# Kernel tuning notes

Measured on AMD Instinct MI355X. Metric: run time of the kernel, lower is better.

Reference implementation:

```python
import jax, jax.numpy as jnp
import numpy as np

N = 16384      # nodes (radar cells x batched graphs)
H = 128        # n_hidden
N_ENV = 7
N_IN = N_ENV + 2 + 1  # env + coords + density = 10
T_CTX = 24
HORIZON = 40
T = T_CTX + HORIZON


def setup_inputs() -> dict:
    key = jax.random.key(0)
    ks = jax.random.split(key, 40)

    def w(k, shape, fan_in):
        return jax.random.normal(k, shape, jnp.float32) * np.float32(1.0 / np.sqrt(fan_in))

    inp = {}
    inp["x"] = jax.random.normal(ks[0], (N, T), jnp.float32)
    inp["coords"] = jax.random.normal(ks[1], (N, 2), jnp.float32)
    inp["env"] = jax.random.normal(ks[2], (N, N_ENV, T), jnp.float32)
    # --- encoder params ---
    inp["enc_W_in"] = w(ks[3], (H, N_IN), N_IN)           # Linear(n_in->H), no bias
    inp["enc_Wih0"] = w(ks[4], (4 * H, H), H)
    inp["enc_Whh0"] = w(ks[5], (4 * H, H), H)
    inp["enc_bih0"] = jnp.zeros((4 * H,), jnp.float32)
    inp["enc_bhh0"] = jnp.zeros((4 * H,), jnp.float32)
    inp["enc_Wih1"] = w(ks[6], (4 * H, H), H)
    inp["enc_Whh1"] = w(ks[7], (4 * H, H), H)
    inp["enc_bih1"] = jnp.zeros((4 * H,), jnp.float32)
    inp["enc_bhh1"] = jnp.zeros((4 * H,), jnp.float32)
    # --- NodeLSTM params ---
    inp["node_W_in"] = w(ks[8], (H, N_IN), N_IN)          # Linear(n_in->H), no bias
    inp["in_Wih"] = w(ks[9], (4 * H, 2 * H), 2 * H)       # lstm_in takes [inputs, enc_state]
    inp["in_Whh"] = w(ks[10], (4 * H, H), H)
    inp["in_bih"] = jnp.zeros((4 * H,), jnp.float32)
    inp["in_bhh"] = jnp.zeros((4 * H,), jnp.float32)
    inp["l1_Wih"] = w(ks[11], (4 * H, H), H)
    inp["l1_Whh"] = w(ks[12], (4 * H, H), H)
    inp["l1_bih"] = jnp.zeros((4 * H,), jnp.float32)
    inp["l1_bhh"] = jnp.zeros((4 * H,), jnp.float32)
    # hidden2in / hidden2out heads: Linear(H,H) -> ReLU -> Linear(H,1)
    inp["h2in_W1"] = w(ks[13], (H, H), H)
    inp["h2in_b1"] = jnp.zeros((H,), jnp.float32)
    inp["h2in_W2"] = w(ks[14], (1, H), H)
    inp["h2in_b2"] = jnp.zeros((1,), jnp.float32)
    inp["h2out_W1"] = w(ks[15], (H, H), H)
    inp["h2out_b1"] = jnp.zeros((H,), jnp.float32)
    inp["h2out_W2"] = w(ks[16], (1, H), H)
    inp["h2out_b2"] = jnp.zeros((1,), jnp.float32)
    return inp


def _lstm_cell(xin, h, c, Wih, Whh, bih, bhh):
    # torch.nn.LSTMCell semantics; gate order i, f, g, o
    gates = xin @ Wih.T + h @ Whh.T + (bih + bhh)
    i, f, g, o = jnp.split(gates, 4, axis=1)
    c_new = jax.nn.sigmoid(f) * c + jax.nn.sigmoid(i) * jnp.tanh(g)
    h_new = jax.nn.sigmoid(o) * jnp.tanh(c_new)
    return h_new, c_new


def reference(x, coords, env,
              enc_W_in, enc_Wih0, enc_Whh0, enc_bih0, enc_bhh0,
              enc_Wih1, enc_Whh1, enc_bih1, enc_bhh1,
              node_W_in, in_Wih, in_Whh, in_bih, in_bhh,
              l1_Wih, l1_Whh, l1_bih, l1_bhh,
              h2in_W1, h2in_b1, h2in_W2, h2in_b2,
              h2out_W1, h2out_b1, h2out_W2, h2out_b2):
    n = x.shape[0]
    z = jnp.zeros((n, H), x.dtype)

    # ---------- encoder: scan over T_CTX context steps ----------
    def enc_step(carry, xs):
        h0, c0, h1, c1 = carry
        xt, et = xs  # [N], [N, N_ENV]
        inp = jnp.concatenate([xt[:, None], coords, et], axis=1) @ enc_W_in.T
        h0, c0 = _lstm_cell(inp, h0, c0, enc_Wih0, enc_Whh0, enc_bih0, enc_bhh0)
        h1, c1 = _lstm_cell(h0, h1, c1, enc_Wih1, enc_Whh1, enc_bih1, enc_bhh1)
        return (h0, c0, h1, c1), None

    enc_xs = (x[:, :T_CTX].T, jnp.moveaxis(env[:, :, :T_CTX], 2, 0))
    (h0, c0, h1, c1), _ = jax.lax.scan(enc_step, (z, z, z, z), enc_xs)
    enc_state = h1  # h[-1] captured at setup_states, fixed over the horizon

    def head(hid, W1, b1, W2, b2):
        return jax.nn.sigmoid(jax.nn.relu(hid @ W1.T + b1) @ W2.T + b2)

    # ---------- decoder: scan over HORIZON forecast steps ----------
    def dec_step(carry, et):
        xc, h0, c0, h1, c1 = carry
        inp = jnp.concatenate([xc, coords, et], axis=1) @ node_W_in.T
        inp = jnp.concatenate([inp, enc_state], axis=1)  # [N, 2H]
        h0, c0 = _lstm_cell(inp, h0, c0, in_Wih, in_Whh, in_bih, in_bhh)
        h1, c1 = _lstm_cell(h0, h1, c1, l1_Wih, l1_Whh, l1_bih, l1_bhh)
        x_in = head(h1, h2in_W1, h2in_b1, h2in_W2, h2in_b2)
        x_out = head(h1, h2out_W1, h2out_b1, h2out_W2, h2out_b2)
        xn = xc + x_in - x_out * xc  # source/sink update, [N, 1]
        return (xn, h0, c0, h1, c1), xn

    x0 = x[:, T_CTX - 1][:, None]
    dec_xs = jnp.moveaxis(env[:, :, T_CTX:T_CTX + HORIZON], 2, 0)
    _, ys = jax.lax.scan(dec_step, (x0, h0, c0, h1, c1), dec_xs)  # [HORIZON, N, 1]
    return jnp.transpose(ys[..., 0], (1, 0))  # [N, HORIZON]
```

## Files before the change

kernel.cpp:

```cpp
#include <hip/hip_runtime.h>
#include <hip/hip_bf16.h>
#include <cstdint>
#include <cstddef>

typedef __bf16 bf16_t;
typedef bf16_t bf16x8 __attribute__((ext_vector_type(8)));
typedef bf16_t bf16x4 __attribute__((ext_vector_type(4)));
typedef float  f32x4  __attribute__((ext_vector_type(4)));
typedef unsigned short u16x8 __attribute__((ext_vector_type(8)));

#define TT    64
#define T_CTX 24
#define HOR   40
#define SA    264
#define NTH   512
#define EWS   132

#define MFMA __builtin_amdgcn_mfma_f32_16x16x32_bf16

#define O_PKE   16
#define O_PKD   (O_PKE + 262144)
#define O_PKX   (O_PKD + 294912)
#define O_BIAS  (O_PKX + 131072)
#define O_HEADP (O_BIAS + 2048)
#define O_WINE  (O_HEADP + 512)
#define O_WINN  (O_WINE + 1536)
#define O_B2    (O_WINN + 1536)

struct Ptrs { const void* q[29]; };

__device__ __forceinline__ float sigm(float x) {
  return __builtin_amdgcn_rcpf(1.f + __expf(-x));
}
__device__ __forceinline__ float tanh_(float x) {
  return 1.f - 2.f * __builtin_amdgcn_rcpf(1.f + __expf(2.f * x));
}
__device__ __forceinline__ unsigned pk2(float a, float b) {
  unsigned ua = __float_as_uint(a), ub = __float_as_uint(b);
  ua = (ua + 0x7fffu + ((ua >> 16) & 1u)) >> 16;
  ub = (ub + 0x7fffu + ((ub >> 16) & 1u)) >> 16;
  return ua | (ub << 16);
}
__device__ __forceinline__ float uplo(unsigned p){ return __uint_as_float(p << 16); }
__device__ __forceinline__ float uphi(unsigned p){ return __uint_as_float(p & 0xffff0000u); }

__global__ void detect_kernel(const unsigned short* __restrict__ wsrc, int* __restrict__ flag)
{
  int tid = threadIdx.x;
  int wild = 0;
  for (int i = tid; i < 256; i += 64) {
    unsigned short b = wsrc[i];
    float v  = __uint_as_float(((unsigned)b) << 16);
    float av = fabsf(v);
    unsigned e = (b >> 7) & 0xff;
    if (av > 1000.f || e == 0xff || (((b & 0x7fff) != 0) && av < 1e-9f)) wild++;
  }
  for (int off = 32; off; off >>= 1) wild += __shfl_down(wild, off, 64);
  if (tid == 0) flag[0] = (wild > 16) ? 1 : 0;
}

__global__ void prep_kernel(Ptrs P, bf16_t* __restrict__ wb, const int* __restrict__ flag)
{
  const bool f32 = (flag[0] != 0);
  const int gtid = blockIdx.x * blockDim.x + threadIdx.x;
  const int gsz  = gridDim.x * blockDim.x;
  auto rd = [&](const void* src, int i) -> float {
    return f32 ? ((const float*)src)[i] : (float)((const bf16_t*)src)[i];
  };

  for (int i = gtid; i < 262144; i += gsz) {
    int w = i >> 15, r = i & 32767, f = r >> 9, e = r & 511;
    int ln = e >> 3, j = e & 7;
    int seg = f >> 5, fk = f & 31, kt = fk >> 2, g = fk & 3;
    int row = g * 128 + w * 16 + (ln & 15);
    int col = kt * 32 + ((ln >> 4) << 3) + j;
    float v;
    if (seg == 0) v = (col < 128) ? rd(P.q[4], row * 128 + col) : rd(P.q[5], row * 128 + col - 128);
    else          v = (col < 128) ? rd(P.q[8], row * 128 + col) : rd(P.q[9], row * 128 + col - 128);
    wb[O_PKE + i] = (bf16_t)v;
  }
  for (int i = gtid; i < 294912; i += gsz) {
    int w = i / 36864, r = i - w * 36864, f = r >> 9, e = r & 511;
    int ln = e >> 3, j = e & 7;
    int colk = ((ln >> 4) << 3) + j;
    float v;
    if (f < 64) {
      int seg = f >> 5, fk = f & 31, kt = fk >> 2, g = fk & 3;
      int row = g * 128 + w * 16 + (ln & 15);
      int col = kt * 32 + colk;
      if (seg == 0) v = (col < 128) ? rd(P.q[13], row * 256 + col) : rd(P.q[14], row * 128 + col - 128);
      else          v = (col < 128) ? rd(P.q[17], row * 128 + col) : rd(P.q[18], row * 128 + col - 128);
    } else {
      int f2 = f - 64, h = f2 >> 2, kt = f2 & 3;
      int row = w * 16 + (ln & 15);
      int col = kt * 32 + colk;
      v = rd(h ? P.q[25] : P.q[21], row * 128 + col);
    }
    wb[O_PKD + i] = (bf16_t)v;
  }
  for (int i = gtid; i < 131072; i += gsz) {
    int w = i >> 14, r = i & 16383, f = r >> 9, e = r & 511;
    int ln = e >> 3, j = e & 7;
    int kt = f >> 2, g = f & 3;
    int row = g * 128 + w * 16 + (ln & 15);
    int col = kt * 32 + ((ln >> 4) << 3) + j;
    wb[O_PKX + i] = (bf16_t)rd(P.q[13], row * 256 + 128 + col);
  }
  for (int i = gtid; i < 512; i += gsz) {
    wb[O_BIAS + i]        = (bf16_t)(rd(P.q[6],  i) + rd(P.q[7],  i));
    wb[O_BIAS + 512 + i]  = (bf16_t)(rd(P.q[10], i) + rd(P.q[11], i));
    wb[O_BIAS + 1024 + i] = (bf16_t)(rd(P.q[15], i) + rd(P.q[16], i));
    wb[O_BIAS + 1536 + i] = (bf16_t)(rd(P.q[19], i) + rd(P.q[20], i));
  }
  for (int i = gtid; i < 128; i += gsz) {
    wb[O_HEADP + i]       = (bf16_t)rd(P.q[22], i);
    wb[O_HEADP + 128 + i] = (bf16_t)rd(P.q[23], i);
    wb[O_HEADP + 256 + i] = (bf16_t)rd(P.q[26], i);
    wb[O_HEADP + 384 + i] = (bf16_t)rd(P.q[27], i);
  }
  for (int i = gtid; i < 1536; i += gsz) {
    int cc = i / 12, j = i % 12;
    wb[O_WINE + i] = (j < 10) ? (bf16_t)rd(P.q[3],  cc * 10 + j) : (bf16_t)0.f;
    wb[O_WINN + i] = (j < 10) ? (bf16_t)rd(P.q[12], cc * 10 + j) : (bf16_t)0.f;
  }
  if (gtid == 0) {
    wb[O_B2]     = (bf16_t)rd(P.q[24], 0);
    wb[O_B2 + 1] = (bf16_t)rd(P.q[28], 0);
  }
}

struct PreB { bf16x8 b[2][4]; };

__device__ __forceinline__ PreB preB(const bf16_t* __restrict__ pl) {
  PreB r;
#pragma unroll
  for (int p = 0; p < 2; ++p)
#pragma unroll
    for (int g = 0; g < 4; ++g)
      r.b[p][g] = *(const bf16x8*)(pl + (p * 4 + g) * 512);
  return r;
}

template<int NKT>
__device__ __forceinline__ void gemm_pk(f32x4 (&acc)[4][4], const bf16_t* __restrict__ As,
                                        const bf16_t* __restrict__ pl, const PreB& pre,
                                        const bf16_t* __restrict__ plpf, PreB* __restrict__ pf,
                                        int l, int q)
{
  bf16x8 bw[3][4];
#pragma unroll
  for (int g = 0; g < 4; ++g) { bw[0][g] = pre.b[0][g]; bw[1][g] = pre.b[1][g]; }
#pragma unroll
  for (int g = 0; g < 4; ++g) bw[2][g] = *(const bf16x8*)(pl + (8 + g) * 512);
#pragma unroll
  for (int kt = 0; kt < NKT; ++kt) {
    if (kt == 1) {
#pragma unroll
      for (int p = 0; p < 2; ++p)
#pragma unroll
        for (int g = 0; g < 4; ++g)
          pf->b[p][g] = *(const bf16x8*)(plpf + (p * 4 + g) * 512);
    }
    const bf16_t* Ar = As + l * SA + kt * 32 + q * 8;
    bf16x8 a0 = *(const bf16x8*)(Ar);
    bf16x8 a1 = *(const bf16x8*)(Ar + 16 * SA);
#pragma unroll
    for (int g = 0; g < 4; ++g) acc[g][0] = MFMA(a0, bw[kt % 3][g], acc[g][0], 0, 0, 0);
    a0 = *(const bf16x8*)(Ar + 32 * SA);
#pragma unroll
    for (int g = 0; g < 4; ++g) acc[g][1] = MFMA(a1, bw[kt % 3][g], acc[g][1], 0, 0, 0);
    a1 = *(const bf16x8*)(Ar + 48 * SA);
#pragma unroll
    for (int g = 0; g < 4; ++g) acc[g][2] = MFMA(a0, bw[kt % 3][g], acc[g][2], 0, 0, 0);
#pragma unroll
    for (int g = 0; g < 4; ++g) acc[g][3] = MFMA(a1, bw[kt % 3][g], acc[g][3], 0, 0, 0);
    if (kt + 3 < NKT) {
#pragma unroll
      for (int g = 0; g < 4; ++g)
        bw[kt % 3][g] = *(const bf16x8*)(pl + ((kt + 3) * 4 + g) * 512);
    }
  }
}

template<bool DUAL>
__device__ __forceinline__ void cell_up(f32x4 (&acc)[4][4], float (&c)[16],
                                        bf16_t* __restrict__ shb, bf16_t* __restrict__ sha,
                                        const bf16_t* __restrict__ bias,
                                        int wid, int l, int q)
{
  const int jc = wid * 16 + l;
  const float bi  = (float)bias[jc];
  const float bf_ = (float)bias[128 + jc];
  const float bg  = (float)bias[256 + jc];
  const float bo  = (float)bias[384 + jc];
#pragma unroll
  for (int mt = 0; mt < 4; ++mt) {
#pragma unroll
    for (int r = 0; r < 4; ++r) {
      float gi = acc[0][mt][r] + bi;
      float gf = acc[1][mt][r] + bf_;
      float gg = acc[2][mt][r] + bg;
      float go = acc[3][mt][r] + bo;
      float cn = sigm(gf) * c[mt * 4 + r] + sigm(gi) * tanh_(gg);
      float hh = sigm(go) * tanh_(cn);
      c[mt * 4 + r] = cn;
      const int row = mt * 16 + q * 4 + r;
      shb[row * SA + jc] = (bf16_t)hh;
      if (DUAL) sha[row * SA + jc] = (bf16_t)hh;
    }
  }
}

__device__ __forceinline__ void proj16(const float* v, const bf16_t* __restrict__ wbase,
                                       bf16_t* __restrict__ sx, int nd, int sub)
{
  bf16x8 o0, o1;
#pragma unroll
  for (int cc = 0; cc < 16; ++cc) {
    const bf16_t* wr = wbase + (sub * 16 + cc) * 12;
    bf16x4 w0 = *(const bf16x4*)(wr);
    bf16x4 w1 = *(const bf16x4*)(wr + 4);
    bf16x4 w2 = *(const bf16x4*)(wr + 8);
    float a = v[0] * (float)w0[0] + v[1] * (float)w0[1] + v[2] * (float)w0[2] + v[3] * (float)w0[3]
            + v[4] * (float)w1[0] + v[5] * (float)w1[1] + v[6] * (float)w1[2] + v[7] * (float)w1[3]
            + v[8] * (float)w2[0] + v[9] * (float)w2[1];
    if (cc < 8) o0[cc] = (bf16_t)a; else o1[cc - 8] = (bf16_t)a;
  }
  *(bf16x8*)(sx + nd * SA + sub * 16)     = o0;
  *(bf16x8*)(sx + nd * SA + sub * 16 + 8) = o1;
}

template<typename T>
__global__ __launch_bounds__(NTH, 2) void lstm_persist(
    const T* __restrict__ x, const T* __restrict__ coords, const T* __restrict__ env,
    const bf16_t* __restrict__ w, const int* __restrict__ flag, T* __restrict__ out)
{
  const bool want_f32 = (sizeof(T) == 4);
  if ((flag[0] != 0) != want_f32) return;

  __shared__ __align__(16) bf16_t bufA[64 * SA];
  __shared__ __align__(16) bf16_t bufB[64 * SA];
  __shared__ __align__(16) bf16_t s_win[2 * 128 * 12];
  __shared__ __align__(16) bf16_t s_bias[4 * 512];
  __shared__ float s_red[128];
  __shared__ float s_xc[64];
  __shared__ __align__(16) float s_ew[64 * EWS];
  __shared__ float s_out[64 * HOR];

  const int tid  = threadIdx.x;
  const int wid  = tid >> 6;
  const int lane = tid & 63;
  const int l    = tid & 15;
  const int q    = (tid & 63) >> 4;
  const int node0 = blockIdx.x * 64;
  const int nd  = tid >> 3;
  const int sub = tid & 7;
  const int nd_e = tid / 7;
  const int e_e  = tid - nd_e * 7;

  const bf16_t* plE0 = w + O_PKE + wid * 32768 + lane * 8;
  const bf16_t* plE1 = plE0 + 16384;
  const bf16_t* plD0 = w + O_PKD + wid * 36864 + lane * 8;
  const bf16_t* plD1 = plD0 + 16384;
  const bf16_t* plH  = plD0 + 32768;
  const bf16_t* plX  = w + O_PKX + wid * 16384 + lane * 8;

  auto load_ew = [&](int t0) {
    float* dst = (tid < 448) ? &s_ew[nd_e * EWS + e_e * 16]
                             : &s_ew[(tid - 448) * EWS + 112];
    const T* src = (tid < 448) ? env + ((size_t)(node0 + nd_e) * 7 + e_e) * TT + t0
                               : x + (size_t)(node0 + tid - 448) * TT + t0;
    if constexpr (sizeof(T) == 4) {
#pragma unroll
      for (int u = 0; u < 4; ++u) {
        f32x4 vv = __builtin_nontemporal_load((const f32x4*)src + u);
        *((f32x4*)dst + u) = vv;
      }
    } else {
#pragma unroll
      for (int u = 0; u < 2; ++u) {
        u16x8 vv = __builtin_nontemporal_load((const u16x8*)src + u);
#pragma unroll
        for (int k = 0; k < 8; ++k)
          dst[u * 8 + k] = __uint_as_float(((unsigned)vv[k]) << 16);
      }
    }
  };

  for (int i = tid; i < 2048; i += NTH) s_bias[i] = w[O_BIAS + i];
  for (int i = tid; i < 3072; i += NTH) s_win[i]  = w[O_WINE + i];
  for (int i = tid; i < 64 * SA; i += NTH) { bufA[i] = (bf16_t)0.f; bufB[i] = (bf16_t)0.f; }
  load_ew(0);

  const float cx = (float)coords[(size_t)(node0 + nd) * 2 + 0];
  const float cy = (float)coords[(size_t)(node0 + nd) * 2 + 1];

  float c0[16], c1[16];
#pragma unroll
  for (int i = 0; i < 16; ++i) { c0[i] = 0.f; c1[i] = 0.f; }

  PreB pA = preB(plE0);
  PreB pD;
  __syncthreads();

#pragma unroll 1
  for (int t = 0; t < T_CTX; ++t) {
    if (t == 16) { __syncthreads(); load_ew(16); __syncthreads(); }
    const int tw = t & 15;
    float v[10];
    v[0] = s_ew[nd * EWS + 112 + tw];
    v[1] = cx; v[2] = cy;
#pragma unroll
    for (int e = 0; e < 7; ++e) v[3 + e] = s_ew[nd * EWS + e * 16 + tw];
    proj16(v, s_win, bufA, nd, sub);
    __syncthreads();

    f32x4 acc[4][4];
#pragma unroll
    for (int g = 0; g < 4; ++g)
#pragma unroll
      for (int mt = 0; mt < 4; ++mt) acc[g][mt] = f32x4{0.f, 0.f, 0.f, 0.f};
    PreB pC;
    gemm_pk<8>(acc, bufA, plE0, pA, plE1, &pC, l, q);
    __syncthreads();
    cell_up<true>(acc, c0, bufB, bufA + 128, s_bias, wid, l, q);
    __syncthreads();

#pragma unroll
    for (int g = 0; g < 4; ++g)
#pragma unroll
      for (int mt = 0; mt < 4; ++mt) acc[g][mt] = f32x4{0.f, 0.f, 0.f, 0.f};
    gemm_pk<8>(acc, bufB, plE1, pC, (t < T_CTX - 1) ? plE0 : plX, &pA, l, q);
    __syncthreads();
    cell_up<false>(acc, c1, bufB + 128, nullptr, s_bias + 512, wid, l, q);
  }
  __syncthreads();

  uint2 geh[4][4];
  {
    f32x4 acc[4][4];
#pragma unroll
    for (int g = 0; g < 4; ++g)
#pragma unroll
      for (int mt = 0; mt < 4; ++mt) acc[g][mt] = f32x4{0.f, 0.f, 0.f, 0.f};
    gemm_pk<4>(acc, bufB + 128, plX, pA, plD0, &pD, l, q);
#pragma unroll
    for (int g = 0; g < 4; ++g)
#pragma unroll
      for (int mt = 0; mt < 4; ++mt)
        geh[g][mt] = uint2{pk2(acc[g][mt][0], acc[g][mt][1]),
                           pk2(acc[g][mt][2], acc[g][mt][3])};
  }
  if (tid < 64) s_xc[tid] = s_ew[tid * EWS + 112 + 7];
  const float b2i = (float)w[O_B2];
  const float b2o = (float)w[O_B2 + 1];
  const float b1i = (float)w[O_HEADP + wid * 16 + l];
  const float w2i = (float)w[O_HEADP + 128 + wid * 16 + l];
  const float b1o = (float)w[O_HEADP + 256 + wid * 16 + l];
  const float w2o = (float)w[O_HEADP + 384 + wid * 16 + l];
  __syncthreads();

#pragma unroll 1
  for (int s = 0; s < HOR; ++s) {
    const int t = T_CTX + s;
    if ((t & 15) == 0) { load_ew(t); __syncthreads(); }
    const int tw = t & 15;
    float v[10];
    v[0] = s_xc[nd];
    v[1] = cx; v[2] = cy;
#pragma unroll
    for (int e = 0; e < 7; ++e) v[3 + e] = s_ew[nd * EWS + e * 16 + tw];
    proj16(v, s_win + 1536, bufA, nd, sub);
    __syncthreads();

    f32x4 acc[4][4];
#pragma unroll
    for (int g = 0; g < 4; ++g)
#pragma unroll
      for (int mt = 0; mt < 4; ++mt)
        acc[g][mt] = f32x4{uplo(geh[g][mt].x), uphi(geh[g][mt].x),
                           uplo(geh[g][mt].y), uphi(geh[g][mt].y)};
    PreB pC;
    gemm_pk<8>(acc, bufA, plD0, pD, plD1, &pC, l, q);
    __syncthreads();
    cell_up<true>(acc, c0, bufB, bufA + 128, s_bias + 1024, wid, l, q);
    __syncthreads();

#pragma unroll
    for (int g = 0; g < 4; ++g)
#pragma unroll
      for (int mt = 0; mt < 4; ++mt) acc[g][mt] = f32x4{0.f, 0.f, 0.f, 0.f};
    gemm_pk<8>(acc, bufB, plD1, pC, plD0, &pD, l, q);
    bf16x8 hb[8];
#pragma unroll
    for (int f = 0; f < 8; ++f) hb[f] = *(const bf16x8*)(plH + f * 512);
    __syncthreads();
    cell_up<false>(acc, c1, bufB + 128, nullptr, s_bias + 1536, wid, l, q);
    if (tid < 128) s_red[tid] = 0.f;
    __syncthreads();

    f32x4 hacc[2][4];
#pragma unroll
    for (int hd = 0; hd < 2; ++hd)
#pragma unroll
      for (int mt = 0; mt < 4; ++mt) hacc[hd][mt] = f32x4{0.f, 0.f, 0.f, 0.f};
#pragma unroll
    for (int kt = 0; kt < 4; ++kt) {
      bf16x8 a[4];
#pragma unroll
      for (int mt = 0; mt < 4; ++mt)
        a[mt] = *(const bf16x8*)(bufB + 128 + (mt * 16 + l) * SA + kt * 32 + q * 8);
#pragma unroll
      for (int mt = 0; mt < 4; ++mt) {
        hacc[0][mt] = MFMA(a[mt], hb[kt],     hacc[0][mt], 0, 0, 0);
        hacc[1][mt] = MFMA(a[mt], hb[4 + kt], hacc[1][mt], 0, 0, 0);
      }
    }
#pragma unroll
    for (int hd = 0; hd < 2; ++hd) {
      const float b1v = hd ? b1o : b1i;
      const float w2v = hd ? w2o : w2i;
#pragma unroll
      for (int mt = 0; mt < 4; ++mt)
#pragma unroll
        for (int r = 0; r < 4; ++r) {
          float val = fmaxf(hacc[hd][mt][r] + b1v, 0.f) * w2v;
          val += __shfl_xor(val, 1, 64);
          val += __shfl_xor(val, 2, 64);
          val += __shfl_xor(val, 4, 64);
          val += __shfl_xor(val, 8, 64);
          if (l == 0) atomicAdd(&s_red[hd * 64 + mt * 16 + q * 4 + r], val);
        }
    }
    __syncthreads();
    if (tid < 64) {
      float xc = s_xc[tid];
      float si = sigm(s_red[tid] + b2i);
      float so = sigm(s_red[64 + tid] + b2o);
      float xn = xc + si - so * xc;
      s_xc[tid] = xn;
      s_out[tid * HOR + s] = xn;
    }
    __syncthreads();
  }

  for (int i = tid; i < 64 * HOR; i += NTH)
    out[(size_t)node0 * HOR + i] = (T)s_out[i];
}

extern "C" void kernel_launch(void* const* d_in, const int* in_sizes, int n_in,
                              void* d_out, int out_size, void* d_ws, size_t ws_size,
                              hipStream_t stream) {
  (void)in_sizes; (void)n_in; (void)out_size; (void)ws_size;
  Ptrs P;
  for (int i = 0; i < 29; ++i) P.q[i] = d_in[i];
  int*    flag = (int*)d_ws;
  bf16_t* w    = (bf16_t*)d_ws;

  detect_kernel<<<1, 64, 0, stream>>>((const unsigned short*)d_in[4], flag);
  prep_kernel<<<256, 256, 0, stream>>>(P, w, flag);
  lstm_persist<float><<<256, NTH, 0, stream>>>(
      (const float*)d_in[0], (const float*)d_in[1], (const float*)d_in[2],
      w, flag, (float*)d_out);
  lstm_persist<bf16_t><<<256, NTH, 0, stream>>>(
      (const bf16_t*)d_in[0], (const bf16_t*)d_in[1], (const bf16_t*)d_in[2],
      w, flag, (bf16_t*)d_out);
}
```

Measured before the change: 1.933 ms.

## Process 128 nodes per 1024-thread block sharing weight fragments across row halves

Doubles the nodes per workgroup to 128 using 16 waves, where two groups of 8 waves split the rows and share the same weight column slices. The grid drops to 128 blocks. The 16-step env staging buffer is replaced by a per-step double-buffered scalar load, and outputs are written directly to global each step instead of staged in shared memory. The aim is to halve weight traffic per node and cut shared memory for the env buffer. The risk is that with 128 blocks on 256 CUs only half the CUs are used, and the per-step scalar global loads add latency on every iteration.

```diff
diff --git a/kernel.cpp b/kernel.cpp
--- a/kernel.cpp
+++ b/kernel.cpp
@@ -7,14 +7,13 @@
 typedef bf16_t bf16x8 __attribute__((ext_vector_type(8)));
 typedef bf16_t bf16x4 __attribute__((ext_vector_type(4)));
 typedef float  f32x4  __attribute__((ext_vector_type(4)));
-typedef unsigned short u16x8 __attribute__((ext_vector_type(8)));
 
 #define TT    64
 #define T_CTX 24
 #define HOR   40
 #define SA    264
-#define NTH   512
-#define EWS   132
+#define NTH   1024
+#define NODES 128
 
 #define MFMA __builtin_amdgcn_mfma_f32_16x16x32_bf16
 
@@ -186,9 +185,8 @@
 __device__ __forceinline__ void cell_up(f32x4 (&acc)[4][4], float (&c)[16],
                                         bf16_t* __restrict__ shb, bf16_t* __restrict__ sha,
                                         const bf16_t* __restrict__ bias,
-                                        int wid, int l, int q)
-{
-  const int jc = wid * 16 + l;
+                                        int jc, int l, int q)
+{
   const float bi  = (float)bias[jc];
   const float bf_ = (float)bias[128 + jc];
   const float bg  = (float)bias[256 + jc];
@@ -231,66 +229,51 @@
 }
 
 template<typename T>
-__global__ __launch_bounds__(NTH, 2) void lstm_persist(
+__global__ __launch_bounds__(NTH, 1) void lstm_persist(
     const T* __restrict__ x, const T* __restrict__ coords, const T* __restrict__ env,
     const bf16_t* __restrict__ w, const int* __restrict__ flag, T* __restrict__ out)
 {
   const bool want_f32 = (sizeof(T) == 4);
   if ((flag[0] != 0) != want_f32) return;
 
-  __shared__ __align__(16) bf16_t bufA[64 * SA];
-  __shared__ __align__(16) bf16_t bufB[64 * SA];
+  __shared__ __align__(16) bf16_t bufA[NODES * SA];
+  __shared__ __align__(16) bf16_t bufB[NODES * SA];
   __shared__ __align__(16) bf16_t s_win[2 * 128 * 12];
   __shared__ __align__(16) bf16_t s_bias[4 * 512];
-  __shared__ float s_red[128];
-  __shared__ float s_xc[64];
-  __shared__ __align__(16) float s_ew[64 * EWS];
-  __shared__ float s_out[64 * HOR];
+  __shared__ float s_red[2 * NODES];
+  __shared__ float s_xc[NODES];
+  __shared__ float s_env[2][NODES][8];
 
   const int tid  = threadIdx.x;
   const int wid  = tid >> 6;
+  const int ws   = wid & 7;
+  const int rb   = (wid >> 3) * 64;
   const int lane = tid & 63;
   const int l    = tid & 15;
   const int q    = (tid & 63) >> 4;
-  const int node0 = blockIdx.x * 64;
+  const int jc   = ws * 16 + l;
+  const int node0 = blockIdx.x * NODES;
   const int nd  = tid >> 3;
   const int sub = tid & 7;
   const int nd_e = tid / 7;
   const int e_e  = tid - nd_e * 7;
 
-  const bf16_t* plE0 = w + O_PKE + wid * 32768 + lane * 8;
+  const bf16_t* plE0 = w + O_PKE + ws * 32768 + lane * 8;
   const bf16_t* plE1 = plE0 + 16384;
-  const bf16_t* plD0 = w + O_PKD + wid * 36864 + lane * 8;
+  const bf16_t* plD0 = w + O_PKD + ws * 36864 + lane * 8;
   const bf16_t* plD1 = plD0 + 16384;
   const bf16_t* plH  = plD0 + 32768;
-  const bf16_t* plX  = w + O_PKX + wid * 16384 + lane * 8;
-
-  auto load_ew = [&](int t0) {
-    float* dst = (tid < 448) ? &s_ew[nd_e * EWS + e_e * 16]
-                             : &s_ew[(tid - 448) * EWS + 112];
-    const T* src = (tid < 448) ? env + ((size_t)(node0 + nd_e) * 7 + e_e) * TT + t0
-                               : x + (size_t)(node0 + tid - 448) * TT + t0;
-    if constexpr (sizeof(T) == 4) {
-#pragma unroll
-      for (int u = 0; u < 4; ++u) {
-        f32x4 vv = __builtin_nontemporal_load((const f32x4*)src + u);
-        *((f32x4*)dst + u) = vv;
-      }
-    } else {
-#pragma unroll
-      for (int u = 0; u < 2; ++u) {
-        u16x8 vv = __builtin_nontemporal_load((const u16x8*)src + u);
-#pragma unroll
-        for (int k = 0; k < 8; ++k)
-          dst[u * 8 + k] = __uint_as_float(((unsigned)vv[k]) << 16);
-      }
-    }
+  const bf16_t* plX  = w + O_PKX + ws * 16384 + lane * 8;
+
+  auto load_env = [&](int t0, int buf) {
+    if (tid < 896) s_env[buf][nd_e][e_e] = (float)env[((size_t)(node0 + nd_e) * 7 + e_e) * TT + t0];
+    else           s_env[buf][tid - 896][7] = (float)x[(size_t)(node0 + tid - 896) * TT + t0];
   };
 
   for (int i = tid; i < 2048; i += NTH) s_bias[i] = w[O_BIAS + i];
   for (int i = tid; i < 3072; i += NTH) s_win[i]  = w[O_WINE + i];
-  for (int i = tid; i < 64 * SA; i += NTH) { bufA[i] = (bf16_t)0.f; bufB[i] = (bf16_t)0.f; }
-  load_ew(0);
+  for (int i = tid; i < NODES * SA; i += NTH) { bufA[i] = (bf16_t)0.f; bufB[i] = (bf16_t)0.f; }
+  load_env(0, 0);
 
   const float cx = (float)coords[(size_t)(node0 + nd) * 2 + 0];
   const float cy = (float)coords[(size_t)(node0 + nd) * 2 + 1];
@@ -305,14 +288,14 @@
 
 #pragma unroll 1
   for (int t = 0; t < T_CTX; ++t) {
-    if (t == 16) { __syncthreads(); load_ew(16); __syncthreads(); }
-    const int tw = t & 15;
+    const int tn = t + 1;
     float v[10];
-    v[0] = s_ew[nd * EWS + 112 + tw];
+    v[0] = s_env[t & 1][nd][7];
     v[1] = cx; v[2] = cy;
 #pragma unroll
-    for (int e = 0; e < 7; ++e) v[3 + e] = s_ew[nd * EWS + e * 16 + tw];
+    for (int e = 0; e < 7; ++e) v[3 + e] = s_env[t & 1][nd][e];
     proj16(v, s_win, bufA, nd, sub);
+    load_env(tn, tn & 1);
     __syncthreads();
 
     f32x4 acc[4][4];
@@ -321,18 +304,18 @@
 #pragma unroll
       for (int mt = 0; mt < 4; ++mt) acc[g][mt] = f32x4{0.f, 0.f, 0.f, 0.f};
     PreB pC;
-    gemm_pk<8>(acc, bufA, plE0, pA, plE1, &pC, l, q);
-    __syncthreads();
-    cell_up<true>(acc, c0, bufB, bufA + 128, s_bias, wid, l, q);
+    gemm_pk<8>(acc, bufA + rb * SA, plE0, pA, plE1, &pC, l, q);
+    __syncthreads();
+    cell_up<true>(acc, c0, bufB + rb * SA, bufA + rb * SA + 128, s_bias, jc, l, q);
     __syncthreads();
 
 #pragma unroll
     for (int g = 0; g < 4; ++g)
 #pragma unroll
       for (int mt = 0; mt < 4; ++mt) acc[g][mt] = f32x4{0.f, 0.f, 0.f, 0.f};
-    gemm_pk<8>(acc, bufB, plE1, pC, (t < T_CTX - 1) ? plE0 : plX, &pA, l, q);
-    __syncthreads();
-    cell_up<false>(acc, c1, bufB + 128, nullptr, s_bias + 512, wid, l, q);
+    gemm_pk<8>(acc, bufB + rb * SA, plE1, pC, (t < T_CTX - 1) ? plE0 : plX, &pA, l, q);
+    __syncthreads();
+    cell_up<false>(acc, c1, bufB + rb * SA + 128, nullptr, s_bias + 512, jc, l, q);
   }
   __syncthreads();
 
@@ -343,7 +326,7 @@
     for (int g = 0; g < 4; ++g)
 #pragma unroll
       for (int mt = 0; mt < 4; ++mt) acc[g][mt] = f32x4{0.f, 0.f, 0.f, 0.f};
-    gemm_pk<4>(acc, bufB + 128, plX, pA, plD0, &pD, l, q);
+    gemm_pk<4>(acc, bufB + rb * SA + 128, plX, pA, plD0, &pD, l, q);
 #pragma unroll
     for (int g = 0; g < 4; ++g)
 #pragma unroll
@@ -351,26 +334,26 @@
         geh[g][mt] = uint2{pk2(acc[g][mt][0], acc[g][mt][1]),
                            pk2(acc[g][mt][2], acc[g][mt][3])};
   }
-  if (tid < 64) s_xc[tid] = s_ew[tid * EWS + 112 + 7];
+  if (tid < NODES) s_xc[tid] = s_env[1][tid][7];
   const float b2i = (float)w[O_B2];
   const float b2o = (float)w[O_B2 + 1];
-  const float b1i = (float)w[O_HEADP + wid * 16 + l];
-  const float w2i = (float)w[O_HEADP + 128 + wid * 16 + l];
-  const float b1o = (float)w[O_HEADP + 256 + wid * 16 + l];
-  const float w2o = (float)w[O_HEADP + 384 + wid * 16 + l];
+  const float b1i = (float)w[O_HEADP + jc];
+  const float w2i = (float)w[O_HEADP + 128 + jc];
+  const float b1o = (float)w[O_HEADP + 256 + jc];
+  const float w2o = (float)w[O_HEADP + 384 + jc];
   __syncthreads();
 
 #pragma unroll 1
   for (int s = 0; s < HOR; ++s) {
     const int t = T_CTX + s;
-    if ((t & 15) == 0) { load_ew(t); __syncthreads(); }
-    const int tw = t & 15;
+    const int tn = t + 1;
     float v[10];
     v[0] = s_xc[nd];
     v[1] = cx; v[2] = cy;
 #pragma unroll
-    for (int e = 0; e < 7; ++e) v[3 + e] = s_ew[nd * EWS + e * 16 + tw];
+    for (int e = 0; e < 7; ++e) v[3 + e] = s_env[t & 1][nd][e];
     proj16(v, s_win + 1536, bufA, nd, sub);
+    if (tn < TT) load_env(tn, tn & 1);
     __syncthreads();
 
     f32x4 acc[4][4];
@@ -381,22 +364,22 @@
         acc[g][mt] = f32x4{uplo(geh[g][mt].x), uphi(geh[g][mt].x),
                            uplo(geh[g][mt].y), uphi(geh[g][mt].y)};
     PreB pC;
-    gemm_pk<8>(acc, bufA, plD0, pD, plD1, &pC, l, q);
-    __syncthreads();
-    cell_up<true>(acc, c0, bufB, bufA + 128, s_bias + 1024, wid, l, q);
+    gemm_pk<8>(acc, bufA + rb * SA, plD0, pD, plD1, &pC, l, q);
+    __syncthreads();
+    cell_up<true>(acc, c0, bufB + rb * SA, bufA + rb * SA + 128, s_bias + 1024, jc, l, q);
     __syncthreads();
 
 #pragma unroll
     for (int g = 0; g < 4; ++g)
 #pragma unroll
       for (int mt = 0; mt < 4; ++mt) acc[g][mt] = f32x4{0.f, 0.f, 0.f, 0.f};
-    gemm_pk<8>(acc, bufB, plD1, pC, plD0, &pD, l, q);
+    gemm_pk<8>(acc, bufB + rb * SA, plD1, pC, plD0, &pD, l, q);
     bf16x8 hb[8];
 #pragma unroll
     for (int f = 0; f < 8; ++f) hb[f] = *(const bf16x8*)(plH + f * 512);
     __syncthreads();
-    cell_up<false>(acc, c1, bufB + 128, nullptr, s_bias + 1536, wid, l, q);
-    if (tid < 128) s_red[tid] = 0.f;
+    cell_up<false>(acc, c1, bufB + rb * SA + 128, nullptr, s_bias + 1536, jc, l, q);
+    if (tid < 2 * NODES) s_red[tid] = 0.f;
     __syncthreads();
 
     f32x4 hacc[2][4];
@@ -409,7 +392,7 @@
       bf16x8 a[4];
 #pragma unroll
       for (int mt = 0; mt < 4; ++mt)
-        a[mt] = *(const bf16x8*)(bufB + 128 + (mt * 16 + l) * SA + kt * 32 + q * 8);
+        a[mt] = *(const bf16x8*)(bufB + (rb + mt * 16 + l) * SA + 128 + kt * 32 + q * 8);
 #pragma unroll
       for (int mt = 0; mt < 4; ++mt) {
         hacc[0][mt] = MFMA(a[mt], hb[kt],     hacc[0][mt], 0, 0, 0);
@@ -429,23 +412,20 @@
           val += __shfl_xor(val, 2, 64);
           val += __shfl_xor(val, 4, 64);
           val += __shfl_xor(val, 8, 64);
-          if (l == 0) atomicAdd(&s_red[hd * 64 + mt * 16 + q * 4 + r], val);
+          if (l == 0) atomicAdd(&s_red[hd * NODES + rb + mt * 16 + q * 4 + r], val);
         }
     }
     __syncthreads();
-    if (tid < 64) {
+    if (tid < NODES) {
       float xc = s_xc[tid];
       float si = sigm(s_red[tid] + b2i);
-      float so = sigm(s_red[64 + tid] + b2o);
+      float so = sigm(s_red[NODES + tid] + b2o);
       float xn = xc + si - so * xc;
       s_xc[tid] = xn;
-      s_out[tid * HOR + s] = xn;
-    }
-    __syncthreads();
-  }
-
-  for (int i = tid; i < 64 * HOR; i += NTH)
-    out[(size_t)node0 * HOR + i] = (T)s_out[i];
+      out[(size_t)(node0 + tid) * HOR + s] = (T)xn;
+    }
+    __syncthreads();
+  }
 }
 
 extern "C" void kernel_launch(void* const* d_in, const int* in_sizes, int n_in,
@@ -459,10 +439,10 @@
 
   detect_kernel<<<1, 64, 0, stream>>>((const unsigned short*)d_in[4], flag);
   prep_kernel<<<256, 256, 0, stream>>>(P, w, flag);
-  lstm_persist<float><<<256, NTH, 0, stream>>>(
+  lstm_persist<float><<<128, NTH, 0, stream>>>(
       (const float*)d_in[0], (const float*)d_in[1], (const float*)d_in[2],
       w, flag, (float*)d_out);
-  lstm_persist<bf16_t><<<256, NTH, 0, stream>>>(
+  lstm_persist<bf16_t><<<128, NTH, 0, stream>>>(
       (const bf16_t*)d_in[0], (const bf16_t*)d_in[1], (const bf16_t*)d_in[2],
       w, flag, (bf16_t*)d_out);
 }
```

After: 4.846 ms. +150.7%, slower.
